# Optimization experiments

Hardware: AMD Instinct MI355X
Metric: run time of the kernel (lower is better)

Reference implementation:

```python
import jax, jax.numpy as jnp
import numpy as np

HEADS = 8
DIM_HEAD = 64
SCALE = DIM_HEAD ** -0.5


def setup_inputs() -> dict:
    key = jax.random.key(0)
    ks = jax.random.split(key, 6)
    B, N, M = 4, 4096, 1024
    QD, CD, ID = 320, 768, 512
    s = lambda d: (1.0 / np.sqrt(d)).astype(np.float32)
    return {
        "x": jax.random.normal(ks[0], (B, N, QD), dtype=jnp.float32),
        "context": jax.random.normal(ks[1], (B, M, CD), dtype=jnp.float32),
        "Wq": jax.random.normal(ks[2], (QD, ID), dtype=jnp.float32) * s(QD),
        "Wk": jax.random.normal(ks[3], (CD, ID), dtype=jnp.float32) * s(CD),
        "Wv": jax.random.normal(ks[4], (CD, ID), dtype=jnp.float32) * s(CD),
        "Wo": jax.random.normal(ks[5], (ID, QD), dtype=jnp.float32) * s(ID),
        "bo": jnp.zeros((QD,), dtype=jnp.float32),
    }


def reference(x, context, Wq, Wk, Wv, Wo, bo):
    B, N, _ = x.shape
    M = context.shape[1]
    # projections
    q = (x @ Wq).reshape(B, N, HEADS, DIM_HEAD)        # b n h d
    k = (context @ Wk).reshape(B, M, HEADS, DIM_HEAD)  # b m h d
    v = (context @ Wv).reshape(B, M, HEADS, DIM_HEAD)
    # scaled dot-product attention per head
    scores = jnp.einsum("bnhd,bmhd->bhnm", q, k) * SCALE
    attn = jax.nn.softmax(scores, axis=-1)
    out = jnp.einsum("bhnm,bmhd->bnhd", attn, v).reshape(B, N, HEADS * DIM_HEAD)
    # output projection (dropout p=0.0 is identity)
    return out @ Wo + bo
```

## Files before the change

### kernel.cpp

```cpp
#include <hip/hip_runtime.h>
#include <cmath>

constexpr int BATCH  = 4;
constexpr int SEQ_N  = 4096;
constexpr int SEQ_M  = 1024;
constexpr int QD     = 320;
constexpr int CD     = 768;
constexpr int ID     = 512;
constexpr float QFOLD = 0.125f * 1.44269504f;
constexpr float EK2F  = -8.0f * 1.44269504f;

typedef __bf16 bf16x8 __attribute__((ext_vector_type(8)));
typedef __bf16 bf16x4 __attribute__((ext_vector_type(4)));
typedef __bf16 bf16x2 __attribute__((ext_vector_type(2)));
typedef float  f32x4  __attribute__((ext_vector_type(4)));

__device__ __forceinline__ void gload_lds16(const __bf16* g, __bf16* l) {
    __builtin_amdgcn_global_load_lds(
        (const __attribute__((address_space(1))) void*)g,
        (__attribute__((address_space(3))) void*)l, 16, 0, 0);
}

__global__ __launch_bounds__(256)
void cvt_all(const float* __restrict__ x, const float* __restrict__ ctx,
             const float* __restrict__ Wq, const float* __restrict__ Wk,
             const float* __restrict__ Wv, const float* __restrict__ Wo,
             __bf16* __restrict__ xb, __bf16* __restrict__ ctxb,
             __bf16* __restrict__ WqT, __bf16* __restrict__ WkT,
             __bf16* __restrict__ WvT, __bf16* __restrict__ WoT) {
    __shared__ float tile[32][33];
    int bid = blockIdx.x;
    if (bid < 4096) {
        constexpr int NX8 = SEQ_N * BATCH * QD / 8;
        int i = bid * 256 + threadIdx.x;
        const float* s; __bf16* d; int j;
        if (i < NX8) { s = x; d = xb; j = i; }
        else         { s = ctx; d = ctxb; j = i - NX8; }
        const float4* sp = reinterpret_cast<const float4*>(s) + (size_t)j * 2;
        float4 a = sp[0], b = sp[1];
        bf16x8 o = { (__bf16)a.x, (__bf16)a.y, (__bf16)a.z, (__bf16)a.w,
                     (__bf16)b.x, (__bf16)b.y, (__bf16)b.z, (__bf16)b.w };
        reinterpret_cast<bf16x8*>(d)[j] = o;
        return;
    }
    int wb = bid - 4096;
    const float* W; __bf16* WT; int K, N, tid; float scl = 1.0f;
    if (wb < 160)      { W = Wq; WT = WqT; K = 320; N = 512; tid = wb; scl = QFOLD; }
    else if (wb < 544) { W = Wk; WT = WkT; K = 768; N = 512; tid = wb - 160; }
    else if (wb < 928) { W = Wv; WT = WvT; K = 768; N = 512; tid = wb - 544; }
    else               { W = Wo; WT = WoT; K = 512; N = 320; tid = wb - 928; }
    int kt = K / 32;
    int k0 = (tid % kt) * 32, n0 = (tid / kt) * 32;
    int tc = threadIdx.x & 31, tr = threadIdx.x >> 5;
#pragma unroll
    for (int p = 0; p < 4; ++p)
        tile[p * 8 + tr][tc] = W[(size_t)(k0 + p * 8 + tr) * N + n0 + tc];
    __syncthreads();
#pragma unroll
    for (int p = 0; p < 4; ++p)
        WT[(size_t)(n0 + p * 8 + tr) * K + k0 + tc] = (__bf16)(tile[tc][p * 8 + tr] * scl);
}

__global__ __launch_bounds__(256)
void gemm_kv(const __bf16* __restrict__ A, const __bf16* __restrict__ BT,
             __bf16* __restrict__ Kb, __bf16* __restrict__ Vt, int M, int K) {
    __shared__ __attribute__((aligned(16))) __bf16 sA[2][64][64];
    __shared__ __attribute__((aligned(16))) __bf16 sB[2][64][64];

    const int t = threadIdx.x;
    const int wave = t >> 6, lane = t & 63;
    const int q = lane >> 4, c = lane & 15;
    const int wm = wave >> 1, wn = wave & 1;
    const int row0 = blockIdx.x * 64, col0 = blockIdx.y * 64;
    const int srow = lane >> 3, sch = lane & 7;
    const int fch = sch ^ srow;

    auto stage = [&](int buf, int k0) {
#pragma unroll
        for (int i = 0; i < 2; ++i) {
            int r = wave * 16 + i * 8;
            gload_lds16(A + (size_t)(row0 + r + srow) * K + k0 + fch * 8,
                        &sA[buf][r][0] + lane * 8);
            gload_lds16(BT + (size_t)(col0 + r + srow) * K + k0 + fch * 8,
                        &sB[buf][r][0] + lane * 8);
        }
    };

    f32x4 acc[2][2] = {};
    stage(0, 0);
    const int iters = K >> 6;
    for (int it = 0; it < iters; ++it) {
        const int p = it & 1;
        __syncthreads();
        if (it + 1 < iters) stage(p ^ 1, (it + 1) * 64);
#pragma unroll
        for (int ks = 0; ks < 2; ++ks) {
            const int so = ((ks * 4 + q) ^ (c & 7)) * 8;
            bf16x8 am[2], bn[2];
#pragma unroll
            for (int i = 0; i < 2; ++i)
                am[i] = *reinterpret_cast<const bf16x8*>(&sA[p][wm * 32 + i * 16 + c][0] + so);
#pragma unroll
            for (int j = 0; j < 2; ++j)
                bn[j] = *reinterpret_cast<const bf16x8*>(&sB[p][wn * 32 + j * 16 + c][0] + so);
#pragma unroll
            for (int i = 0; i < 2; ++i)
#pragma unroll
                for (int j = 0; j < 2; ++j)
                    acc[i][j] = __builtin_amdgcn_mfma_f32_16x16x32_bf16(bn[j], am[i], acc[i][j], 0, 0, 0);
        }
    }

    if (blockIdx.y < 8) {
#pragma unroll
        for (int i = 0; i < 2; ++i)
#pragma unroll
            for (int j = 0; j < 2; ++j) {
                int mrow = row0 + wm * 32 + i * 16 + c;
                int ncol = col0 + wn * 32 + j * 16 + q * 4;
                bf16x4 v = { (__bf16)acc[i][j][0], (__bf16)acc[i][j][1],
                             (__bf16)acc[i][j][2], (__bf16)acc[i][j][3] };
                *reinterpret_cast<bf16x4*>(&Kb[(size_t)mrow * 512 + ncol]) = v;
            }
    } else {
        __bf16* ldsT = (__bf16*)sA;
        __syncthreads();
#pragma unroll
        for (int i = 0; i < 2; ++i)
#pragma unroll
            for (int j = 0; j < 2; ++j) {
                int ml = wm * 32 + i * 16 + c;
                int dl = wn * 32 + j * 16 + q * 4;
#pragma unroll
                for (int r = 0; r < 4; ++r)
                    ldsT[(dl + r) * 72 + ml] = (__bf16)acc[i][j][r];
            }
        __syncthreads();
        int b = row0 >> 10, m0 = row0 & 1023;
        int h = (col0 - 512) >> 6;
        int d = t >> 2, ch = t & 3;
        __bf16* dst = Vt + (((size_t)((b * 8 + h) * 64 + d)) << 10) + m0 + ch * 16;
        const __bf16* src = &ldsT[d * 72 + ch * 16];
        *reinterpret_cast<bf16x8*>(dst)     = *reinterpret_cast<const bf16x8*>(src);
        *reinterpret_cast<bf16x8*>(dst + 8) = *reinterpret_cast<const bf16x8*>(src + 8);
    }
}

__global__ __launch_bounds__(256, 2)
void flash_attn(const __bf16* __restrict__ xb, const __bf16* __restrict__ WqT,
                const __bf16* __restrict__ Kb, const __bf16* __restrict__ Vt,
                __bf16* __restrict__ AO) {
    __shared__ __attribute__((aligned(16))) __bf16 smem[34816];
    __bf16* sPT = smem + 16384;

    const int t = threadIdx.x;
    const int wave = t >> 6, lane = t & 63;
    const int q = lane >> 4, c = lane & 15;
    const int bh = blockIdx.y;
    const int b = bh >> 3, h = bh & 7;
    const int n0 = blockIdx.x * 256;
    const int srow = lane >> 3, sch = lane & 7;
    const int fch = sch ^ srow;

    f32x4 accQ[4][4] = {};
    {
        __bf16* sX = smem;
        __bf16* sW = smem + 16384;
        for (int k0 = 0; k0 < QD; k0 += 64) {
            __syncthreads();
#pragma unroll
            for (int i = 0; i < 8; ++i) {
                int r = wave * 64 + i * 8;
                gload_lds16(xb + (size_t)(b * SEQ_N + n0 + r + srow) * QD + k0 + fch * 8,
                            sX + r * 64 + lane * 8);
            }
#pragma unroll
            for (int i = 0; i < 2; ++i) {
                int r = wave * 16 + i * 8;
                gload_lds16(WqT + (size_t)(h * 64 + r + srow) * QD + k0 + fch * 8,
                            sW + r * 64 + lane * 8);
            }
            __syncthreads();
#pragma unroll
            for (int ks = 0; ks < 2; ++ks) {
                const int so = ((ks * 4 + q) ^ (c & 7)) * 8;
                bf16x8 aw[4], bx[4];
#pragma unroll
                for (int dt = 0; dt < 4; ++dt)
                    aw[dt] = *reinterpret_cast<const bf16x8*>(sW + (dt * 16 + c) * 64 + so);
#pragma unroll
                for (int qt = 0; qt < 4; ++qt)
                    bx[qt] = *reinterpret_cast<const bf16x8*>(sX + (wave * 64 + qt * 16 + c) * 64 + so);
#pragma unroll
                for (int dt = 0; dt < 4; ++dt)
#pragma unroll
                    for (int qt = 0; qt < 4; ++qt)
                        accQ[dt][qt] = __builtin_amdgcn_mfma_f32_16x16x32_bf16(aw[dt], bx[qt], accQ[dt][qt], 0, 0, 0);
            }
        }
    }
    __syncthreads();

    __bf16* sQw = sPT + wave * 4608;
#pragma unroll
    for (int dt = 0; dt < 4; ++dt)
#pragma unroll
        for (int qt = 0; qt < 4; ++qt) {
            bf16x2 w0 = { (__bf16)accQ[dt][qt][0], (__bf16)accQ[dt][qt][1] };
            bf16x2 w1 = { (__bf16)accQ[dt][qt][2], (__bf16)accQ[dt][qt][3] };
            __bf16* pr = sQw + (qt * 16 + c) * 72 + dt * 16 + q * 4;
            *reinterpret_cast<bf16x2*>(pr)     = w0;
            *reinterpret_cast<bf16x2*>(pr + 2) = w1;
        }
    bf16x8 aq[4][2];
#pragma unroll
    for (int qt = 0; qt < 4; ++qt)
#pragma unroll
        for (int ks = 0; ks < 2; ++ks)
            aq[qt][ks] = *reinterpret_cast<const bf16x8*>(sQw + (qt * 16 + c) * 72 + ks * 32 + q * 8);

    auto stageKV = [&](int buf, int m0) {
        __bf16* sK = smem + buf * 8192;
        __bf16* sV = smem + buf * 8192 + 4096;
#pragma unroll
        for (int i = 0; i < 2; ++i) {
            int r = wave * 16 + i * 8;
            gload_lds16(Kb + (size_t)(b * SEQ_M + m0 + r + srow) * ID + h * 64 + fch * 8,
                        sK + r * 64 + lane * 8);
            gload_lds16(Vt + (((size_t)((b * 8 + h) * 64 + r + srow)) << 10) + m0 + fch * 8,
                        sV + r * 64 + lane * 8);
        }
    };

    const bf16x8 ONES = { (__bf16)1.0f, (__bf16)1.0f, (__bf16)1.0f, (__bf16)1.0f,
                          (__bf16)1.0f, (__bf16)1.0f, (__bf16)1.0f, (__bf16)1.0f };
    f32x4 accO[4][4] = {};
    f32x4 accL[4] = {};

    stageKV(0, 0);
    constexpr int TILES = SEQ_M / 64;
    for (int mt = 0; mt < TILES; ++mt) {
        const int p = mt & 1;
        __syncthreads();
        if (mt + 1 < TILES) stageKV(p ^ 1, (mt + 1) * 64);
        const __bf16* sK = smem + p * 8192;
        const __bf16* sV = smem + p * 8192 + 4096;

        f32x4 s[4][4];
#pragma unroll
        for (int qt = 0; qt < 4; ++qt)
#pragma unroll
            for (int ct = 0; ct < 4; ++ct)
                s[qt][ct] = f32x4{ EK2F, EK2F, EK2F, EK2F };
#pragma unroll
        for (int ks = 0; ks < 2; ++ks) {
            const int so = ((ks * 4 + q) ^ (c & 7)) * 8;
#pragma unroll
            for (int ct = 0; ct < 4; ++ct) {
                bf16x8 ak = *reinterpret_cast<const bf16x8*>(sK + (ct * 16 + c) * 64 + so);
#pragma unroll
                for (int qt = 0; qt < 4; ++qt)
                    s[qt][ct] = __builtin_amdgcn_mfma_f32_16x16x32_bf16(ak, aq[qt][ks], s[qt][ct], 0, 0, 0);
            }
        }

#pragma unroll
        for (int qt = 0; qt < 4; ++qt)
#pragma unroll
            for (int ct = 0; ct < 4; ++ct) {
                float p0 = exp2f(s[qt][ct][0]);
                float p1 = exp2f(s[qt][ct][1]);
                float p2 = exp2f(s[qt][ct][2]);
                float p3 = exp2f(s[qt][ct][3]);
                bf16x2 w0 = { (__bf16)p0, (__bf16)p1 };
                bf16x2 w1 = { (__bf16)p2, (__bf16)p3 };
                __bf16* pr = sQw + (qt * 16 + c) * 72 + ct * 16 + q * 4;
                *reinterpret_cast<bf16x2*>(pr)     = w0;
                *reinterpret_cast<bf16x2*>(pr + 2) = w1;
            }

#pragma unroll
        for (int ks = 0; ks < 2; ++ks) {
            const int so = ((ks * 4 + q) ^ (c & 7)) * 8;
            bf16x8 bp[4];
#pragma unroll
            for (int qt = 0; qt < 4; ++qt)
                bp[qt] = *reinterpret_cast<const bf16x8*>(sQw + (qt * 16 + c) * 72 + ks * 32 + q * 8);
#pragma unroll
            for (int qt = 0; qt < 4; ++qt)
                accL[qt] = __builtin_amdgcn_mfma_f32_16x16x32_bf16(ONES, bp[qt], accL[qt], 0, 0, 0);
#pragma unroll
            for (int nt = 0; nt < 4; ++nt) {
                bf16x8 av = *reinterpret_cast<const bf16x8*>(sV + (nt * 16 + c) * 64 + so);
#pragma unroll
                for (int qt = 0; qt < 4; ++qt)
                    accO[qt][nt] = __builtin_amdgcn_mfma_f32_16x16x32_bf16(av, bp[qt], accO[qt][nt], 0, 0, 0);
            }
        }
    }

#pragma unroll
    for (int qt = 0; qt < 4; ++qt) {
        float inv = 1.0f / accL[qt][0];
        size_t rowb = (size_t)(b * SEQ_N + n0 + wave * 64 + qt * 16 + c) * ID + h * 64;
#pragma unroll
        for (int nt = 0; nt < 4; ++nt) {
            bf16x4 v = { (__bf16)(accO[qt][nt][0] * inv), (__bf16)(accO[qt][nt][1] * inv),
                         (__bf16)(accO[qt][nt][2] * inv), (__bf16)(accO[qt][nt][3] * inv) };
            *reinterpret_cast<bf16x4*>(&AO[rowb + nt * 16 + q * 4]) = v;
        }
    }
}

__global__ __launch_bounds__(256)
void gemm_out(const __bf16* __restrict__ A, const __bf16* __restrict__ BT,
              const float* __restrict__ bias, float* __restrict__ C,
              int M, int N, int K) {
    __shared__ __attribute__((aligned(16))) __bf16 sA[2][128][64];
    __shared__ __attribute__((aligned(16))) __bf16 sB[2][64][64];

    const int t = threadIdx.x;
    const int wave = t >> 6, lane = t & 63;
    const int q = lane >> 4, c = lane & 15;
    const int wm = wave >> 1, wn = wave & 1;
    const int row0 = blockIdx.x * 128, col0 = blockIdx.y * 64;
    const int srow = lane >> 3, sch = lane & 7;
    const int fch = sch ^ srow;

    auto stage = [&](int buf, int k0) {
#pragma unroll
        for (int i = 0; i < 4; ++i) {
            int r = wave * 32 + i * 8;
            gload_lds16(A + (size_t)(row0 + r + srow) * K + k0 + fch * 8,
                        &sA[buf][r][0] + lane * 8);
        }
#pragma unroll
        for (int i = 0; i < 2; ++i) {
            int r = wave * 16 + i * 8;
            gload_lds16(BT + (size_t)(col0 + r + srow) * K + k0 + fch * 8,
                        &sB[buf][r][0] + lane * 8);
        }
    };

    f32x4 acc[4][2] = {};
    stage(0, 0);
    const int iters = K >> 6;
    for (int it = 0; it < iters; ++it) {
        const int p = it & 1;
        __syncthreads();
        if (it + 1 < iters) stage(p ^ 1, (it + 1) * 64);
#pragma unroll
        for (int ks = 0; ks < 2; ++ks) {
            const int so = ((ks * 4 + q) ^ (c & 7)) * 8;
            bf16x8 am[4], bn[2];
#pragma unroll
            for (int i = 0; i < 4; ++i)
                am[i] = *reinterpret_cast<const bf16x8*>(&sA[p][wm * 64 + i * 16 + c][0] + so);
#pragma unroll
            for (int j = 0; j < 2; ++j)
                bn[j] = *reinterpret_cast<const bf16x8*>(&sB[p][wn * 32 + j * 16 + c][0] + so);
#pragma unroll
            for (int i = 0; i < 4; ++i)
#pragma unroll
                for (int j = 0; j < 2; ++j)
                    acc[i][j] = __builtin_amdgcn_mfma_f32_16x16x32_bf16(bn[j], am[i], acc[i][j], 0, 0, 0);
        }
    }

#pragma unroll
    for (int i = 0; i < 4; ++i)
#pragma unroll
        for (int j = 0; j < 2; ++j) {
            int mrow = row0 + wm * 64 + i * 16 + c;
            int ncol = col0 + wn * 32 + j * 16 + q * 4;
            float4 v = { acc[i][j][0] + bias[ncol + 0],
                         acc[i][j][1] + bias[ncol + 1],
                         acc[i][j][2] + bias[ncol + 2],
                         acc[i][j][3] + bias[ncol + 3] };
            *reinterpret_cast<float4*>(&C[(size_t)mrow * N + ncol]) = v;
        }
}

extern "C" void kernel_launch(void* const* d_in, const int* in_sizes, int n_in,
                              void* d_out, int out_size, void* d_ws, size_t ws_size,
                              hipStream_t stream) {
    const float* x   = (const float*)d_in[0];
    const float* ctx = (const float*)d_in[1];
    const float* Wq  = (const float*)d_in[2];
    const float* Wk  = (const float*)d_in[3];
    const float* Wv  = (const float*)d_in[4];
    const float* Wo  = (const float*)d_in[5];
    const float* bo  = (const float*)d_in[6];
    float* out = (float*)d_out;

    char* ws = (char*)d_ws;
    __bf16* xb   = (__bf16*)(ws + 0);
    __bf16* ctxb = (__bf16*)(ws + 10485760);
    __bf16* AO   = (__bf16*)(ws + 16777216);
    __bf16* Kb   = (__bf16*)(ws + 33554432);
    __bf16* Vt   = (__bf16*)(ws + 37748736);
    __bf16* WqT  = (__bf16*)(ws + 41943040);
    __bf16* WkT  = (__bf16*)(ws + 42270720);
    __bf16* WvT  = (__bf16*)(ws + 43057152);
    __bf16* WoT  = (__bf16*)(ws + 43843584);

    const int MX = BATCH * SEQ_N;
    const int MC = BATCH * SEQ_M;
    dim3 blk(256);

    cvt_all<<<dim3(5184), blk, 0, stream>>>(x, ctx, Wq, Wk, Wv, Wo,
                                            xb, ctxb, WqT, WkT, WvT, WoT);

    gemm_kv<<<dim3(MC / 64, 16), blk, 0, stream>>>(ctxb, WkT, Kb, Vt, MC, CD);

    flash_attn<<<dim3(SEQ_N / 256, 32), blk, 0, stream>>>(xb, WqT, Kb, Vt, AO);

    gemm_out<<<dim3(MX / 128, QD / 64), blk, 0, stream>>>(AO, WoT, bo, out, MX, QD, ID);
}
```

Before: 173.7 us.

## Shrink flash-attention blocks to two waves and enlarge KV GEMM tiles

gemm_kv moves from 64x64 to 128x128 tiles with 4x4 accumulators per wave, and its V transpose is now done per wave in LDS. flash_attn now runs 128 threads covering 128 query rows, with a smaller LDS footprint. It drops KV double buffering for a single buffer with syncs around each load, and processes the KV tile in two 32-column halves so the P buffer is narrower. The aim is more resident blocks and better latency hiding from lower LDS use, at the cost of losing the overlap of KV loads with compute. Q projection work per block is also duplicated across more blocks.

```diff
diff --git a/kernel.cpp b/kernel.cpp
--- a/kernel.cpp
+++ b/kernel.cpp
@@ -64,21 +64,21 @@
 __global__ __launch_bounds__(256)
 void gemm_kv(const __bf16* __restrict__ A, const __bf16* __restrict__ BT,
              __bf16* __restrict__ Kb, __bf16* __restrict__ Vt, int M, int K) {
-    __shared__ __attribute__((aligned(16))) __bf16 sA[2][64][64];
-    __shared__ __attribute__((aligned(16))) __bf16 sB[2][64][64];
+    __shared__ __attribute__((aligned(16))) __bf16 sA[2][128][64];
+    __shared__ __attribute__((aligned(16))) __bf16 sB[2][128][64];
 
     const int t = threadIdx.x;
     const int wave = t >> 6, lane = t & 63;
     const int q = lane >> 4, c = lane & 15;
     const int wm = wave >> 1, wn = wave & 1;
-    const int row0 = blockIdx.x * 64, col0 = blockIdx.y * 64;
+    const int row0 = blockIdx.x * 128, col0 = blockIdx.y * 128;
     const int srow = lane >> 3, sch = lane & 7;
     const int fch = sch ^ srow;
 
     auto stage = [&](int buf, int k0) {
 #pragma unroll
-        for (int i = 0; i < 2; ++i) {
-            int r = wave * 16 + i * 8;
+        for (int i = 0; i < 4; ++i) {
+            int r = wave * 32 + i * 8;
             gload_lds16(A + (size_t)(row0 + r + srow) * K + k0 + fch * 8,
                         &sA[buf][r][0] + lane * 8);
             gload_lds16(BT + (size_t)(col0 + r + srow) * K + k0 + fch * 8,
@@ -86,7 +86,7 @@
         }
     };
 
-    f32x4 acc[2][2] = {};
+    f32x4 acc[4][4] = {};
     stage(0, 0);
     const int iters = K >> 6;
     for (int it = 0; it < iters; ++it) {
@@ -96,76 +96,82 @@
 #pragma unroll
         for (int ks = 0; ks < 2; ++ks) {
             const int so = ((ks * 4 + q) ^ (c & 7)) * 8;
-            bf16x8 am[2], bn[2];
-#pragma unroll
-            for (int i = 0; i < 2; ++i)
-                am[i] = *reinterpret_cast<const bf16x8*>(&sA[p][wm * 32 + i * 16 + c][0] + so);
-#pragma unroll
-            for (int j = 0; j < 2; ++j)
-                bn[j] = *reinterpret_cast<const bf16x8*>(&sB[p][wn * 32 + j * 16 + c][0] + so);
-#pragma unroll
-            for (int i = 0; i < 2; ++i)
-#pragma unroll
-                for (int j = 0; j < 2; ++j)
+            bf16x8 am[4], bn[4];
+#pragma unroll
+            for (int i = 0; i < 4; ++i)
+                am[i] = *reinterpret_cast<const bf16x8*>(&sA[p][wm * 64 + i * 16 + c][0] + so);
+#pragma unroll
+            for (int j = 0; j < 4; ++j)
+                bn[j] = *reinterpret_cast<const bf16x8*>(&sB[p][wn * 64 + j * 16 + c][0] + so);
+#pragma unroll
+            for (int i = 0; i < 4; ++i)
+#pragma unroll
+                for (int j = 0; j < 4; ++j)
                     acc[i][j] = __builtin_amdgcn_mfma_f32_16x16x32_bf16(bn[j], am[i], acc[i][j], 0, 0, 0);
         }
     }
 
-    if (blockIdx.y < 8) {
-#pragma unroll
-        for (int i = 0; i < 2; ++i)
-#pragma unroll
-            for (int j = 0; j < 2; ++j) {
-                int mrow = row0 + wm * 32 + i * 16 + c;
-                int ncol = col0 + wn * 32 + j * 16 + q * 4;
+    if (blockIdx.y < 4) {
+#pragma unroll
+        for (int i = 0; i < 4; ++i)
+#pragma unroll
+            for (int j = 0; j < 4; ++j) {
+                int mrow = row0 + wm * 64 + i * 16 + c;
+                int ncol = col0 + wn * 64 + j * 16 + q * 4;
                 bf16x4 v = { (__bf16)acc[i][j][0], (__bf16)acc[i][j][1],
                              (__bf16)acc[i][j][2], (__bf16)acc[i][j][3] };
                 *reinterpret_cast<bf16x4*>(&Kb[(size_t)mrow * 512 + ncol]) = v;
             }
     } else {
-        __bf16* ldsT = (__bf16*)sA;
         __syncthreads();
-#pragma unroll
-        for (int i = 0; i < 2; ++i)
-#pragma unroll
-            for (int j = 0; j < 2; ++j) {
-                int ml = wm * 32 + i * 16 + c;
-                int dl = wn * 32 + j * 16 + q * 4;
+        __bf16* ldsT = ((__bf16*)sA) + wave * 4608;
+#pragma unroll
+        for (int i = 0; i < 4; ++i)
+#pragma unroll
+            for (int j = 0; j < 4; ++j)
 #pragma unroll
                 for (int r = 0; r < 4; ++r)
-                    ldsT[(dl + r) * 72 + ml] = (__bf16)acc[i][j][r];
-            }
-        __syncthreads();
-        int b = row0 >> 10, m0 = row0 & 1023;
-        int h = (col0 - 512) >> 6;
-        int d = t >> 2, ch = t & 3;
-        __bf16* dst = Vt + (((size_t)((b * 8 + h) * 64 + d)) << 10) + m0 + ch * 16;
-        const __bf16* src = &ldsT[d * 72 + ch * 16];
-        *reinterpret_cast<bf16x8*>(dst)     = *reinterpret_cast<const bf16x8*>(src);
-        *reinterpret_cast<bf16x8*>(dst + 8) = *reinterpret_cast<const bf16x8*>(src + 8);
-    }
-}
-
-__global__ __launch_bounds__(256, 2)
+                    ldsT[(j * 16 + q * 4 + r) * 72 + i * 16 + c] = (__bf16)acc[i][j][r];
+        int b = row0 >> 10;
+        int mcol = (row0 & 1023) + wm * 64;
+        int dbase = col0 - 512 + wn * 64;
+#pragma unroll
+        for (int it = 0; it < 8; ++it) {
+            int dloc = it * 8 + (lane >> 3);
+            int ch = lane & 7;
+            int dg = dbase + dloc;
+            int h = dg >> 6, d = dg & 63;
+            *reinterpret_cast<bf16x8*>(
+                Vt + (((size_t)((b * 8 + h) * 64 + d)) << 10) + mcol + ch * 8) =
+                *reinterpret_cast<const bf16x8*>(&ldsT[dloc * 72 + ch * 8]);
+        }
+    }
+}
+
+__global__ __launch_bounds__(128, 2)
 void flash_attn(const __bf16* __restrict__ xb, const __bf16* __restrict__ WqT,
                 const __bf16* __restrict__ Kb, const __bf16* __restrict__ Vt,
                 __bf16* __restrict__ AO) {
-    __shared__ __attribute__((aligned(16))) __bf16 smem[34816];
-    __bf16* sPT = smem + 16384;
+    __shared__ __attribute__((aligned(16))) __bf16 smem[13312];
+    __bf16* sK  = smem;
+    __bf16* sV  = smem + 4096;
+    __bf16* sPT = smem + 8192;
 
     const int t = threadIdx.x;
     const int wave = t >> 6, lane = t & 63;
     const int q = lane >> 4, c = lane & 15;
     const int bh = blockIdx.y;
     const int b = bh >> 3, h = bh & 7;
-    const int n0 = blockIdx.x * 256;
+    const int n0 = blockIdx.x * 128;
     const int srow = lane >> 3, sch = lane & 7;
     const int fch = sch ^ srow;
+
+    __bf16* sQw = sPT + wave * 2560;
 
     f32x4 accQ[4][4] = {};
     {
         __bf16* sX = smem;
-        __bf16* sW = smem + 16384;
+        __bf16* sW = smem + 8192;
         for (int k0 = 0; k0 < QD; k0 += 64) {
             __syncthreads();
 #pragma unroll
@@ -175,8 +181,8 @@
                             sX + r * 64 + lane * 8);
             }
 #pragma unroll
-            for (int i = 0; i < 2; ++i) {
-                int r = wave * 16 + i * 8;
+            for (int i = 0; i < 4; ++i) {
+                int r = wave * 32 + i * 8;
                 gload_lds16(WqT + (size_t)(h * 64 + r + srow) * QD + k0 + fch * 8,
                             sW + r * 64 + lane * 8);
             }
@@ -201,30 +207,30 @@
     }
     __syncthreads();
 
-    __bf16* sQw = sPT + wave * 4608;
-#pragma unroll
-    for (int dt = 0; dt < 4; ++dt)
-#pragma unroll
-        for (int qt = 0; qt < 4; ++qt) {
-            bf16x2 w0 = { (__bf16)accQ[dt][qt][0], (__bf16)accQ[dt][qt][1] };
-            bf16x2 w1 = { (__bf16)accQ[dt][qt][2], (__bf16)accQ[dt][qt][3] };
-            __bf16* pr = sQw + (qt * 16 + c) * 72 + dt * 16 + q * 4;
-            *reinterpret_cast<bf16x2*>(pr)     = w0;
-            *reinterpret_cast<bf16x2*>(pr + 2) = w1;
-        }
     bf16x8 aq[4][2];
 #pragma unroll
-    for (int qt = 0; qt < 4; ++qt)
-#pragma unroll
-        for (int ks = 0; ks < 2; ++ks)
-            aq[qt][ks] = *reinterpret_cast<const bf16x8*>(sQw + (qt * 16 + c) * 72 + ks * 32 + q * 8);
-
-    auto stageKV = [&](int buf, int m0) {
-        __bf16* sK = smem + buf * 8192;
-        __bf16* sV = smem + buf * 8192 + 4096;
-#pragma unroll
-        for (int i = 0; i < 2; ++i) {
-            int r = wave * 16 + i * 8;
+    for (int ks = 0; ks < 2; ++ks) {
+#pragma unroll
+        for (int cti = 0; cti < 2; ++cti) {
+            int dt = ks * 2 + cti;
+#pragma unroll
+            for (int qt = 0; qt < 4; ++qt) {
+                bf16x2 w0 = { (__bf16)accQ[dt][qt][0], (__bf16)accQ[dt][qt][1] };
+                bf16x2 w1 = { (__bf16)accQ[dt][qt][2], (__bf16)accQ[dt][qt][3] };
+                __bf16* pr = sQw + (qt * 16 + c) * 40 + cti * 16 + q * 4;
+                *reinterpret_cast<bf16x2*>(pr)     = w0;
+                *reinterpret_cast<bf16x2*>(pr + 2) = w1;
+            }
+        }
+#pragma unroll
+        for (int qt = 0; qt < 4; ++qt)
+            aq[qt][ks] = *reinterpret_cast<const bf16x8*>(sQw + (qt * 16 + c) * 40 + q * 8);
+    }
+
+    auto stageKV = [&](int m0) {
+#pragma unroll
+        for (int i = 0; i < 4; ++i) {
+            int r = wave * 32 + i * 8;
             gload_lds16(Kb + (size_t)(b * SEQ_M + m0 + r + srow) * ID + h * 64 + fch * 8,
                         sK + r * 64 + lane * 8);
             gload_lds16(Vt + (((size_t)((b * 8 + h) * 64 + r + srow)) << 10) + m0 + fch * 8,
@@ -237,61 +243,56 @@
     f32x4 accO[4][4] = {};
     f32x4 accL[4] = {};
 
-    stageKV(0, 0);
-    constexpr int TILES = SEQ_M / 64;
-    for (int mt = 0; mt < TILES; ++mt) {
-        const int p = mt & 1;
+    for (int m0 = 0; m0 < SEQ_M; m0 += 64) {
         __syncthreads();
-        if (mt + 1 < TILES) stageKV(p ^ 1, (mt + 1) * 64);
-        const __bf16* sK = smem + p * 8192;
-        const __bf16* sV = smem + p * 8192 + 4096;
-
-        f32x4 s[4][4];
-#pragma unroll
-        for (int qt = 0; qt < 4; ++qt)
-#pragma unroll
-            for (int ct = 0; ct < 4; ++ct)
-                s[qt][ct] = f32x4{ EK2F, EK2F, EK2F, EK2F };
-#pragma unroll
-        for (int ks = 0; ks < 2; ++ks) {
-            const int so = ((ks * 4 + q) ^ (c & 7)) * 8;
-#pragma unroll
-            for (int ct = 0; ct < 4; ++ct) {
-                bf16x8 ak = *reinterpret_cast<const bf16x8*>(sK + (ct * 16 + c) * 64 + so);
-#pragma unroll
-                for (int qt = 0; qt < 4; ++qt)
-                    s[qt][ct] = __builtin_amdgcn_mfma_f32_16x16x32_bf16(ak, aq[qt][ks], s[qt][ct], 0, 0, 0);
-            }
-        }
-
-#pragma unroll
-        for (int qt = 0; qt < 4; ++qt)
-#pragma unroll
-            for (int ct = 0; ct < 4; ++ct) {
-                float p0 = exp2f(s[qt][ct][0]);
-                float p1 = exp2f(s[qt][ct][1]);
-                float p2 = exp2f(s[qt][ct][2]);
-                float p3 = exp2f(s[qt][ct][3]);
-                bf16x2 w0 = { (__bf16)p0, (__bf16)p1 };
-                bf16x2 w1 = { (__bf16)p2, (__bf16)p3 };
-                __bf16* pr = sQw + (qt * 16 + c) * 72 + ct * 16 + q * 4;
-                *reinterpret_cast<bf16x2*>(pr)     = w0;
-                *reinterpret_cast<bf16x2*>(pr + 2) = w1;
-            }
-
-#pragma unroll
-        for (int ks = 0; ks < 2; ++ks) {
-            const int so = ((ks * 4 + q) ^ (c & 7)) * 8;
+        stageKV(m0);
+        __syncthreads();
+
+#pragma unroll
+        for (int hh = 0; hh < 2; ++hh) {
+            f32x4 s[4][2];
+#pragma unroll
+            for (int qt = 0; qt < 4; ++qt)
+#pragma unroll
+                for (int cti = 0; cti < 2; ++cti)
+                    s[qt][cti] = f32x4{ EK2F, EK2F, EK2F, EK2F };
+#pragma unroll
+            for (int ks = 0; ks < 2; ++ks) {
+                const int so = ((ks * 4 + q) ^ (c & 7)) * 8;
+#pragma unroll
+                for (int cti = 0; cti < 2; ++cti) {
+                    bf16x8 ak = *reinterpret_cast<const bf16x8*>(
+                        sK + ((hh * 2 + cti) * 16 + c) * 64 + so);
+#pragma unroll
+                    for (int qt = 0; qt < 4; ++qt)
+                        s[qt][cti] = __builtin_amdgcn_mfma_f32_16x16x32_bf16(ak, aq[qt][ks], s[qt][cti], 0, 0, 0);
+                }
+            }
+#pragma unroll
+            for (int qt = 0; qt < 4; ++qt)
+#pragma unroll
+                for (int cti = 0; cti < 2; ++cti) {
+                    float p0 = exp2f(s[qt][cti][0]);
+                    float p1 = exp2f(s[qt][cti][1]);
+                    float p2 = exp2f(s[qt][cti][2]);
+                    float p3 = exp2f(s[qt][cti][3]);
+                    bf16x2 w0 = { (__bf16)p0, (__bf16)p1 };
+                    bf16x2 w1 = { (__bf16)p2, (__bf16)p3 };
+                    __bf16* pr = sQw + (qt * 16 + c) * 40 + cti * 16 + q * 4;
+                    *reinterpret_cast<bf16x2*>(pr)     = w0;
+                    *reinterpret_cast<bf16x2*>(pr + 2) = w1;
+                }
+            const int soh = ((hh * 4 + q) ^ (c & 7)) * 8;
             bf16x8 bp[4];
 #pragma unroll
             for (int qt = 0; qt < 4; ++qt)
-                bp[qt] = *reinterpret_cast<const bf16x8*>(sQw + (qt * 16 + c) * 72 + ks * 32 + q * 8);
+                bp[qt] = *reinterpret_cast<const bf16x8*>(sQw + (qt * 16 + c) * 40 + q * 8);
 #pragma unroll
             for (int qt = 0; qt < 4; ++qt)
                 accL[qt] = __builtin_amdgcn_mfma_f32_16x16x32_bf16(ONES, bp[qt], accL[qt], 0, 0, 0);
 #pragma unroll
             for (int nt = 0; nt < 4; ++nt) {
-                bf16x8 av = *reinterpret_cast<const bf16x8*>(sV + (nt * 16 + c) * 64 + so);
+                bf16x8 av = *reinterpret_cast<const bf16x8*>(sV + (nt * 16 + c) * 64 + soh);
 #pragma unroll
                 for (int qt = 0; qt < 4; ++qt)
                     accO[qt][nt] = __builtin_amdgcn_mfma_f32_16x16x32_bf16(av, bp[qt], accO[qt][nt], 0, 0, 0);
@@ -406,14 +407,13 @@
 
     const int MX = BATCH * SEQ_N;
     const int MC = BATCH * SEQ_M;
-    dim3 blk(256);
-
-    cvt_all<<<dim3(5184), blk, 0, stream>>>(x, ctx, Wq, Wk, Wv, Wo,
-                                            xb, ctxb, WqT, WkT, WvT, WoT);
-
-    gemm_kv<<<dim3(MC / 64, 16), blk, 0, stream>>>(ctxb, WkT, Kb, Vt, MC, CD);
-
-    flash_attn<<<dim3(SEQ_N / 256, 32), blk, 0, stream>>>(xb, WqT, Kb, Vt, AO);
-
-    gemm_out<<<dim3(MX / 128, QD / 64), blk, 0, stream>>>(AO, WoT, bo, out, MX, QD, ID);
-}
+
+    cvt_all<<<dim3(5184), dim3(256), 0, stream>>>(x, ctx, Wq, Wk, Wv, Wo,
+                                                  xb, ctxb, WqT, WkT, WvT, WoT);
+
+    gemm_kv<<<dim3(MC / 128, 8), dim3(256), 0, stream>>>(ctxb, WkT, Kb, Vt, MC, CD);
+
+    flash_attn<<<dim3(SEQ_N / 128, 32), dim3(128), 0, stream>>>(xb, WqT, Kb, Vt, AO);
+
+    gemm_out<<<dim3(MX / 128, QD / 64), dim3(256), 0, stream>>>(AO, WoT, bo, out, MX, QD, ID);
+}
```

Result: slower. 182.8 us (+5.2%).

## Split attention KV range across wave pairs with smaller query tiles

Applied to the files above, without the earlier changes.

The flash attention block now covers 128 queries instead of 256. Its four waves form two query halves by two key halves, each pair handling half of every 64-key tile and merging partial outputs and row sums through LDS at the end. Row sums are now computed with scalar adds and shuffles instead of a ones-vector MFMA. The K/V staging is split by role (two waves load K, two load a swizzled V), and launch bounds request 3 blocks per CU with less shared memory. The aim is more blocks and better occupancy, at the cost of an extra LDS reduction, more synchronisation, and recomputing the Q projection twice as often per key stream.

```diff
diff --git a/kernel.cpp b/kernel.cpp
--- a/kernel.cpp
+++ b/kernel.cpp
@@ -12,7 +12,6 @@
 
 typedef __bf16 bf16x8 __attribute__((ext_vector_type(8)));
 typedef __bf16 bf16x4 __attribute__((ext_vector_type(4)));
-typedef __bf16 bf16x2 __attribute__((ext_vector_type(2)));
 typedef float  f32x4  __attribute__((ext_vector_type(4)));
 
 __device__ __forceinline__ void gload_lds16(const __bf16* g, __bf16* l) {
@@ -146,53 +145,53 @@
     }
 }
 
-__global__ __launch_bounds__(256, 2)
+__global__ __launch_bounds__(256, 3)
 void flash_attn(const __bf16* __restrict__ xb, const __bf16* __restrict__ WqT,
                 const __bf16* __restrict__ Kb, const __bf16* __restrict__ Vt,
                 __bf16* __restrict__ AO) {
-    __shared__ __attribute__((aligned(16))) __bf16 smem[34816];
-    __bf16* sPT = smem + 16384;
+    __shared__ __attribute__((aligned(16))) __bf16 smem[26624];
 
     const int t = threadIdx.x;
     const int wave = t >> 6, lane = t & 63;
     const int q = lane >> 4, c = lane & 15;
+    const int qh = wave & 1, kh = wave >> 1;
     const int bh = blockIdx.y;
     const int b = bh >> 3, h = bh & 7;
-    const int n0 = blockIdx.x * 256;
+    const int n0 = blockIdx.x * 128;
     const int srow = lane >> 3, sch = lane & 7;
     const int fch = sch ^ srow;
 
-    f32x4 accQ[4][4] = {};
+    f32x4 accQ[2][4] = {};
     {
         __bf16* sX = smem;
-        __bf16* sW = smem + 16384;
+        __bf16* sW = smem + 8192;
         for (int k0 = 0; k0 < QD; k0 += 64) {
             __syncthreads();
 #pragma unroll
-            for (int i = 0; i < 8; ++i) {
-                int r = wave * 64 + i * 8;
-                gload_lds16(xb + (size_t)(b * SEQ_N + n0 + r + srow) * QD + k0 + fch * 8,
-                            sX + r * 64 + lane * 8);
+            for (int i = 0; i < 4; ++i) {
+                int r = wave * 32 + i * 8 + srow;
+                gload_lds16(xb + (size_t)(b * SEQ_N + n0 + r) * QD + k0 + fch * 8,
+                            sX + (wave * 32 + i * 8) * 64 + lane * 8);
             }
 #pragma unroll
             for (int i = 0; i < 2; ++i) {
-                int r = wave * 16 + i * 8;
-                gload_lds16(WqT + (size_t)(h * 64 + r + srow) * QD + k0 + fch * 8,
-                            sW + r * 64 + lane * 8);
+                int r = wave * 16 + i * 8 + srow;
+                gload_lds16(WqT + (size_t)(h * 64 + r) * QD + k0 + fch * 8,
+                            sW + (wave * 16 + i * 8) * 64 + lane * 8);
             }
             __syncthreads();
 #pragma unroll
             for (int ks = 0; ks < 2; ++ks) {
                 const int so = ((ks * 4 + q) ^ (c & 7)) * 8;
-                bf16x8 aw[4], bx[4];
-#pragma unroll
-                for (int dt = 0; dt < 4; ++dt)
-                    aw[dt] = *reinterpret_cast<const bf16x8*>(sW + (dt * 16 + c) * 64 + so);
+                bf16x8 aw[2], bx[4];
+#pragma unroll
+                for (int dt = 0; dt < 2; ++dt)
+                    aw[dt] = *reinterpret_cast<const bf16x8*>(sW + (kh * 32 + dt * 16 + c) * 64 + so);
 #pragma unroll
                 for (int qt = 0; qt < 4; ++qt)
-                    bx[qt] = *reinterpret_cast<const bf16x8*>(sX + (wave * 64 + qt * 16 + c) * 64 + so);
-#pragma unroll
-                for (int dt = 0; dt < 4; ++dt)
+                    bx[qt] = *reinterpret_cast<const bf16x8*>(sX + (qh * 64 + qt * 16 + c) * 64 + so);
+#pragma unroll
+                for (int dt = 0; dt < 2; ++dt)
 #pragma unroll
                     for (int qt = 0; qt < 4; ++qt)
                         accQ[dt][qt] = __builtin_amdgcn_mfma_f32_16x16x32_bf16(aw[dt], bx[qt], accQ[dt][qt], 0, 0, 0);
@@ -200,63 +199,72 @@
         }
     }
     __syncthreads();
-
-    __bf16* sQw = sPT + wave * 4608;
-#pragma unroll
-    for (int dt = 0; dt < 4; ++dt)
+    __bf16* sQ = smem + 16384;
+#pragma unroll
+    for (int dt = 0; dt < 2; ++dt)
 #pragma unroll
         for (int qt = 0; qt < 4; ++qt) {
-            bf16x2 w0 = { (__bf16)accQ[dt][qt][0], (__bf16)accQ[dt][qt][1] };
-            bf16x2 w1 = { (__bf16)accQ[dt][qt][2], (__bf16)accQ[dt][qt][3] };
-            __bf16* pr = sQw + (qt * 16 + c) * 72 + dt * 16 + q * 4;
-            *reinterpret_cast<bf16x2*>(pr)     = w0;
-            *reinterpret_cast<bf16x2*>(pr + 2) = w1;
-        }
+            bf16x4 v = { (__bf16)accQ[dt][qt][0], (__bf16)accQ[dt][qt][1],
+                         (__bf16)accQ[dt][qt][2], (__bf16)accQ[dt][qt][3] };
+            *reinterpret_cast<bf16x4*>(sQ + (qh * 64 + qt * 16 + c) * 72 + kh * 32 + dt * 16 + q * 4) = v;
+        }
+    __syncthreads();
     bf16x8 aq[4][2];
 #pragma unroll
     for (int qt = 0; qt < 4; ++qt)
 #pragma unroll
         for (int ks = 0; ks < 2; ++ks)
-            aq[qt][ks] = *reinterpret_cast<const bf16x8*>(sQw + (qt * 16 + c) * 72 + ks * 32 + q * 8);
-
-    auto stageKV = [&](int buf, int m0) {
-        __bf16* sK = smem + buf * 8192;
-        __bf16* sV = smem + buf * 8192 + 4096;
-#pragma unroll
-        for (int i = 0; i < 2; ++i) {
-            int r = wave * 16 + i * 8;
-            gload_lds16(Kb + (size_t)(b * SEQ_M + m0 + r + srow) * ID + h * 64 + fch * 8,
-                        sK + r * 64 + lane * 8);
-            gload_lds16(Vt + (((size_t)((b * 8 + h) * 64 + r + srow)) << 10) + m0 + fch * 8,
-                        sV + r * 64 + lane * 8);
+            aq[qt][ks] = *reinterpret_cast<const bf16x8*>(sQ + (qh * 64 + qt * 16 + c) * 72 + ks * 32 + q * 8);
+    __syncthreads();
+
+    auto stageKV = [&](int p, int m0) {
+        __bf16* sK = smem + p * 8192;
+        __bf16* sV = smem + p * 8192 + 4096;
+        if (wave < 2) {
+#pragma unroll
+            for (int i = 0; i < 4; ++i) {
+                int r = wave * 32 + i * 8 + srow;
+                int mg = (r >> 5) * 512 + m0 + (r & 31);
+                gload_lds16(Kb + (size_t)(b * SEQ_M + mg) * ID + h * 64 + fch * 8,
+                            sK + (wave * 32 + i * 8) * 64 + lane * 8);
+            }
+        } else {
+            int v = wave - 2;
+            int sr2 = lane >> 2, sc2 = lane & 3;
+#pragma unroll
+            for (int i = 0; i < 4; ++i) {
+                int rr = v * 64 + i * 16 + sr2;
+                int d = rr & 63, st = rr >> 6;
+                int f2 = sc2 ^ ((rr >> 1) & 3);
+                gload_lds16(Vt + (((size_t)((b * 8 + h) * 64 + d)) << 10) + st * 512 + m0 + f2 * 8,
+                            sV + (v * 64 + i * 16) * 32 + lane * 8);
+            }
         }
     };
 
-    const bf16x8 ONES = { (__bf16)1.0f, (__bf16)1.0f, (__bf16)1.0f, (__bf16)1.0f,
-                          (__bf16)1.0f, (__bf16)1.0f, (__bf16)1.0f, (__bf16)1.0f };
     f32x4 accO[4][4] = {};
-    f32x4 accL[4] = {};
+    float l4[4] = {};
+    __bf16* sPTw = smem + 16384 + wave * 2560;
 
     stageKV(0, 0);
-    constexpr int TILES = SEQ_M / 64;
-    for (int mt = 0; mt < TILES; ++mt) {
+    for (int mt = 0; mt < 16; ++mt) {
         const int p = mt & 1;
         __syncthreads();
-        if (mt + 1 < TILES) stageKV(p ^ 1, (mt + 1) * 64);
-        const __bf16* sK = smem + p * 8192;
-        const __bf16* sV = smem + p * 8192 + 4096;
-
-        f32x4 s[4][4];
+        if (mt + 1 < 16) stageKV(p ^ 1, (mt + 1) * 32);
+        const __bf16* sK = smem + p * 8192 + kh * 2048;
+        const __bf16* sV = smem + p * 8192 + 4096 + kh * 2048;
+
+        f32x4 s[4][2];
 #pragma unroll
         for (int qt = 0; qt < 4; ++qt)
 #pragma unroll
-            for (int ct = 0; ct < 4; ++ct)
+            for (int ct = 0; ct < 2; ++ct)
                 s[qt][ct] = f32x4{ EK2F, EK2F, EK2F, EK2F };
 #pragma unroll
         for (int ks = 0; ks < 2; ++ks) {
             const int so = ((ks * 4 + q) ^ (c & 7)) * 8;
 #pragma unroll
-            for (int ct = 0; ct < 4; ++ct) {
+            for (int ct = 0; ct < 2; ++ct) {
                 bf16x8 ak = *reinterpret_cast<const bf16x8*>(sK + (ct * 16 + c) * 64 + so);
 #pragma unroll
                 for (int qt = 0; qt < 4; ++qt)
@@ -267,47 +275,67 @@
 #pragma unroll
         for (int qt = 0; qt < 4; ++qt)
 #pragma unroll
-            for (int ct = 0; ct < 4; ++ct) {
+            for (int ct = 0; ct < 2; ++ct) {
                 float p0 = exp2f(s[qt][ct][0]);
                 float p1 = exp2f(s[qt][ct][1]);
                 float p2 = exp2f(s[qt][ct][2]);
                 float p3 = exp2f(s[qt][ct][3]);
-                bf16x2 w0 = { (__bf16)p0, (__bf16)p1 };
-                bf16x2 w1 = { (__bf16)p2, (__bf16)p3 };
-                __bf16* pr = sQw + (qt * 16 + c) * 72 + ct * 16 + q * 4;
-                *reinterpret_cast<bf16x2*>(pr)     = w0;
-                *reinterpret_cast<bf16x2*>(pr + 2) = w1;
-            }
-
-#pragma unroll
-        for (int ks = 0; ks < 2; ++ks) {
-            const int so = ((ks * 4 + q) ^ (c & 7)) * 8;
-            bf16x8 bp[4];
+                l4[qt] += (p0 + p1) + (p2 + p3);
+                bf16x4 w = { (__bf16)p0, (__bf16)p1, (__bf16)p2, (__bf16)p3 };
+                *reinterpret_cast<bf16x4*>(sPTw + (qt * 16 + c) * 40 + ct * 16 + q * 4) = w;
+            }
+
+        const int sov = (q ^ ((c >> 1) & 3)) * 8;
+        bf16x8 bp[4];
+#pragma unroll
+        for (int qt = 0; qt < 4; ++qt)
+            bp[qt] = *reinterpret_cast<const bf16x8*>(sPTw + (qt * 16 + c) * 40 + q * 8);
+#pragma unroll
+        for (int nt = 0; nt < 4; ++nt) {
+            bf16x8 av = *reinterpret_cast<const bf16x8*>(sV + (nt * 16 + c) * 32 + sov);
 #pragma unroll
             for (int qt = 0; qt < 4; ++qt)
-                bp[qt] = *reinterpret_cast<const bf16x8*>(sQw + (qt * 16 + c) * 72 + ks * 32 + q * 8);
+                accO[qt][nt] = __builtin_amdgcn_mfma_f32_16x16x32_bf16(av, bp[qt], accO[qt][nt], 0, 0, 0);
+        }
+    }
+
+#pragma unroll
+    for (int qt = 0; qt < 4; ++qt) {
+        l4[qt] += __shfl_xor(l4[qt], 16, 64);
+        l4[qt] += __shfl_xor(l4[qt], 32, 64);
+    }
+    __syncthreads();
+    float* dO = (float*)smem;
+    float* dL = (float*)smem + 8192;
+    if (kh == 1) {
+#pragma unroll
+        for (int qt = 0; qt < 4; ++qt)
+#pragma unroll
+            for (int nt = 0; nt < 4; ++nt)
+#pragma unroll
+                for (int r = 0; r < 4; ++r)
+                    dO[qh * 4096 + qt * 1024 + (nt * 16 + q * 4 + r) * 16 + c] = accO[qt][nt][r];
+        if (q == 0)
 #pragma unroll
             for (int qt = 0; qt < 4; ++qt)
-                accL[qt] = __builtin_amdgcn_mfma_f32_16x16x32_bf16(ONES, bp[qt], accL[qt], 0, 0, 0);
+                dL[qh * 64 + qt * 16 + c] = l4[qt];
+    }
+    __syncthreads();
+    if (kh == 0) {
+#pragma unroll
+        for (int qt = 0; qt < 4; ++qt) {
+            float inv = 1.0f / (l4[qt] + dL[qh * 64 + qt * 16 + c]);
+            size_t rowb = (size_t)(b * SEQ_N + n0 + qh * 64 + qt * 16 + c) * ID + h * 64;
 #pragma unroll
             for (int nt = 0; nt < 4; ++nt) {
-                bf16x8 av = *reinterpret_cast<const bf16x8*>(sV + (nt * 16 + c) * 64 + so);
-#pragma unroll
-                for (int qt = 0; qt < 4; ++qt)
-                    accO[qt][nt] = __builtin_amdgcn_mfma_f32_16x16x32_bf16(av, bp[qt], accO[qt][nt], 0, 0, 0);
-            }
-        }
-    }
-
-#pragma unroll
-    for (int qt = 0; qt < 4; ++qt) {
-        float inv = 1.0f / accL[qt][0];
-        size_t rowb = (size_t)(b * SEQ_N + n0 + wave * 64 + qt * 16 + c) * ID + h * 64;
-#pragma unroll
-        for (int nt = 0; nt < 4; ++nt) {
-            bf16x4 v = { (__bf16)(accO[qt][nt][0] * inv), (__bf16)(accO[qt][nt][1] * inv),
-                         (__bf16)(accO[qt][nt][2] * inv), (__bf16)(accO[qt][nt][3] * inv) };
-            *reinterpret_cast<bf16x4*>(&AO[rowb + nt * 16 + q * 4]) = v;
+                float o0 = accO[qt][nt][0] + dO[qh * 4096 + qt * 1024 + (nt * 16 + q * 4 + 0) * 16 + c];
+                float o1 = accO[qt][nt][1] + dO[qh * 4096 + qt * 1024 + (nt * 16 + q * 4 + 1) * 16 + c];
+                float o2 = accO[qt][nt][2] + dO[qh * 4096 + qt * 1024 + (nt * 16 + q * 4 + 2) * 16 + c];
+                float o3 = accO[qt][nt][3] + dO[qh * 4096 + qt * 1024 + (nt * 16 + q * 4 + 3) * 16 + c];
+                bf16x4 v = { (__bf16)(o0 * inv), (__bf16)(o1 * inv),
+                             (__bf16)(o2 * inv), (__bf16)(o3 * inv) };
+                *reinterpret_cast<bf16x4*>(&AO[rowb + nt * 16 + q * 4]) = v;
+            }
         }
     }
 }
@@ -406,14 +434,13 @@
 
     const int MX = BATCH * SEQ_N;
     const int MC = BATCH * SEQ_M;
-    dim3 blk(256);
-
-    cvt_all<<<dim3(5184), blk, 0, stream>>>(x, ctx, Wq, Wk, Wv, Wo,
-                                            xb, ctxb, WqT, WkT, WvT, WoT);
-
-    gemm_kv<<<dim3(MC / 64, 16), blk, 0, stream>>>(ctxb, WkT, Kb, Vt, MC, CD);
-
-    flash_attn<<<dim3(SEQ_N / 256, 32), blk, 0, stream>>>(xb, WqT, Kb, Vt, AO);
-
-    gemm_out<<<dim3(MX / 128, QD / 64), blk, 0, stream>>>(AO, WoT, bo, out, MX, QD, ID);
-}
+
+    cvt_all<<<dim3(5184), dim3(256), 0, stream>>>(x, ctx, Wq, Wk, Wv, Wo,
+                                                  xb, ctxb, WqT, WkT, WvT, WoT);
+
+    gemm_kv<<<dim3(MC / 64, 16), dim3(256), 0, stream>>>(ctxb, WkT, Kb, Vt, MC, CD);
+
+    flash_attn<<<dim3(SEQ_N / 128, 32), dim3(256), 0, stream>>>(xb, WqT, Kb, Vt, AO);
+
+    gemm_out<<<dim3(MX / 128, QD / 64), dim3(256), 0, stream>>>(AO, WoT, bo, out, MX, QD, ID);
+}
```

New measurement: 227.8 us. 1.31x slower.

## Split attention over two key halves and combine partials in output GEMM

Applied to the files above, without the earlier changes.

Flash attention now launches a second grid dimension that processes half of the context keys each, writing unnormalized bf16 partial outputs and row sums to separate buffers. The output projection GEMM loads both partials, sums them, and normalizes them while staging A into shared memory. The KV staging becomes single-buffered with less LDS, and occupancy is raised to 3 blocks per CU, aiming to fill more CUs. In exchange, the Q projection is computed twice, the partial outputs add global memory traffic, and KV load latency is no longer overlapped.

```diff
diff --git a/kernel.cpp b/kernel.cpp
--- a/kernel.cpp
+++ b/kernel.cpp
@@ -146,12 +146,13 @@
     }
 }
 
-__global__ __launch_bounds__(256, 2)
+__global__ __launch_bounds__(256, 3)
 void flash_attn(const __bf16* __restrict__ xb, const __bf16* __restrict__ WqT,
                 const __bf16* __restrict__ Kb, const __bf16* __restrict__ Vt,
-                __bf16* __restrict__ AO) {
-    __shared__ __attribute__((aligned(16))) __bf16 smem[34816];
-    __bf16* sPT = smem + 16384;
+                __bf16* __restrict__ AO0, __bf16* __restrict__ AO1,
+                float* __restrict__ L0, float* __restrict__ L1) {
+    __shared__ __attribute__((aligned(16))) __bf16 smem[26624];
+    __bf16* sPT = smem + 8192;
 
     const int t = threadIdx.x;
     const int wave = t >> 6, lane = t & 63;
@@ -159,8 +160,12 @@
     const int bh = blockIdx.y;
     const int b = bh >> 3, h = bh & 7;
     const int n0 = blockIdx.x * 256;
+    const int ks2 = blockIdx.z;
     const int srow = lane >> 3, sch = lane & 7;
     const int fch = sch ^ srow;
+
+    __bf16* AOp = ks2 ? AO1 : AO0;
+    float*  Lp  = ks2 ? L1  : L0;
 
     f32x4 accQ[4][4] = {};
     {
@@ -182,8 +187,8 @@
             }
             __syncthreads();
 #pragma unroll
-            for (int ks = 0; ks < 2; ++ks) {
-                const int so = ((ks * 4 + q) ^ (c & 7)) * 8;
+            for (int ksi = 0; ksi < 2; ++ksi) {
+                const int so = ((ksi * 4 + q) ^ (c & 7)) * 8;
                 bf16x8 aw[4], bx[4];
 #pragma unroll
                 for (int dt = 0; dt < 4; ++dt)
@@ -216,19 +221,17 @@
 #pragma unroll
     for (int qt = 0; qt < 4; ++qt)
 #pragma unroll
-        for (int ks = 0; ks < 2; ++ks)
-            aq[qt][ks] = *reinterpret_cast<const bf16x8*>(sQw + (qt * 16 + c) * 72 + ks * 32 + q * 8);
-
-    auto stageKV = [&](int buf, int m0) {
-        __bf16* sK = smem + buf * 8192;
-        __bf16* sV = smem + buf * 8192 + 4096;
+        for (int ksi = 0; ksi < 2; ++ksi)
+            aq[qt][ksi] = *reinterpret_cast<const bf16x8*>(sQw + (qt * 16 + c) * 72 + ksi * 32 + q * 8);
+
+    auto stageKV = [&](int m0) {
 #pragma unroll
         for (int i = 0; i < 2; ++i) {
             int r = wave * 16 + i * 8;
             gload_lds16(Kb + (size_t)(b * SEQ_M + m0 + r + srow) * ID + h * 64 + fch * 8,
-                        sK + r * 64 + lane * 8);
+                        smem + r * 64 + lane * 8);
             gload_lds16(Vt + (((size_t)((b * 8 + h) * 64 + r + srow)) << 10) + m0 + fch * 8,
-                        sV + r * 64 + lane * 8);
+                        smem + 4096 + r * 64 + lane * 8);
         }
     };
 
@@ -237,14 +240,14 @@
     f32x4 accO[4][4] = {};
     f32x4 accL[4] = {};
 
-    stageKV(0, 0);
-    constexpr int TILES = SEQ_M / 64;
-    for (int mt = 0; mt < TILES; ++mt) {
-        const int p = mt & 1;
-        __syncthreads();
-        if (mt + 1 < TILES) stageKV(p ^ 1, (mt + 1) * 64);
-        const __bf16* sK = smem + p * 8192;
-        const __bf16* sV = smem + p * 8192 + 4096;
+    const __bf16* sK = smem;
+    const __bf16* sV = smem + 4096;
+
+    for (int mt = 0; mt < 8; ++mt) {
+        const int m0 = ks2 * 512 + mt * 64;
+        __syncthreads();
+        stageKV(m0);
+        __syncthreads();
 
         f32x4 s[4][4];
 #pragma unroll
@@ -253,14 +256,14 @@
             for (int ct = 0; ct < 4; ++ct)
                 s[qt][ct] = f32x4{ EK2F, EK2F, EK2F, EK2F };
 #pragma unroll
-        for (int ks = 0; ks < 2; ++ks) {
-            const int so = ((ks * 4 + q) ^ (c & 7)) * 8;
+        for (int ksi = 0; ksi < 2; ++ksi) {
+            const int so = ((ksi * 4 + q) ^ (c & 7)) * 8;
 #pragma unroll
             for (int ct = 0; ct < 4; ++ct) {
                 bf16x8 ak = *reinterpret_cast<const bf16x8*>(sK + (ct * 16 + c) * 64 + so);
 #pragma unroll
                 for (int qt = 0; qt < 4; ++qt)
-                    s[qt][ct] = __builtin_amdgcn_mfma_f32_16x16x32_bf16(ak, aq[qt][ks], s[qt][ct], 0, 0, 0);
+                    s[qt][ct] = __builtin_amdgcn_mfma_f32_16x16x32_bf16(ak, aq[qt][ksi], s[qt][ct], 0, 0, 0);
             }
         }
 
@@ -280,12 +283,12 @@
             }
 
 #pragma unroll
-        for (int ks = 0; ks < 2; ++ks) {
-            const int so = ((ks * 4 + q) ^ (c & 7)) * 8;
+        for (int ksi = 0; ksi < 2; ++ksi) {
+            const int so = ((ksi * 4 + q) ^ (c & 7)) * 8;
             bf16x8 bp[4];
 #pragma unroll
             for (int qt = 0; qt < 4; ++qt)
-                bp[qt] = *reinterpret_cast<const bf16x8*>(sQw + (qt * 16 + c) * 72 + ks * 32 + q * 8);
+                bp[qt] = *reinterpret_cast<const bf16x8*>(sQw + (qt * 16 + c) * 72 + ksi * 32 + q * 8);
 #pragma unroll
             for (int qt = 0; qt < 4; ++qt)
                 accL[qt] = __builtin_amdgcn_mfma_f32_16x16x32_bf16(ONES, bp[qt], accL[qt], 0, 0, 0);
@@ -301,21 +304,24 @@
 
 #pragma unroll
     for (int qt = 0; qt < 4; ++qt) {
-        float inv = 1.0f / accL[qt][0];
-        size_t rowb = (size_t)(b * SEQ_N + n0 + wave * 64 + qt * 16 + c) * ID + h * 64;
+        int row = n0 + wave * 64 + qt * 16 + c;
+        if (q == 0)
+            Lp[(size_t)(b * SEQ_N + row) * 8 + h] = accL[qt][0];
+        size_t rowb = (size_t)(b * SEQ_N + row) * ID + h * 64;
 #pragma unroll
         for (int nt = 0; nt < 4; ++nt) {
-            bf16x4 v = { (__bf16)(accO[qt][nt][0] * inv), (__bf16)(accO[qt][nt][1] * inv),
-                         (__bf16)(accO[qt][nt][2] * inv), (__bf16)(accO[qt][nt][3] * inv) };
-            *reinterpret_cast<bf16x4*>(&AO[rowb + nt * 16 + q * 4]) = v;
+            bf16x4 v = { (__bf16)accO[qt][nt][0], (__bf16)accO[qt][nt][1],
+                         (__bf16)accO[qt][nt][2], (__bf16)accO[qt][nt][3] };
+            *reinterpret_cast<bf16x4*>(&AOp[rowb + nt * 16 + q * 4]) = v;
         }
     }
 }
 
 __global__ __launch_bounds__(256)
-void gemm_out(const __bf16* __restrict__ A, const __bf16* __restrict__ BT,
-              const float* __restrict__ bias, float* __restrict__ C,
-              int M, int N, int K) {
+void gemm_out(const __bf16* __restrict__ AO0, const __bf16* __restrict__ AO1,
+              const float* __restrict__ L0, const float* __restrict__ L1,
+              const __bf16* __restrict__ BT, const float* __restrict__ bias,
+              float* __restrict__ C, int M, int N, int K) {
     __shared__ __attribute__((aligned(16))) __bf16 sA[2][128][64];
     __shared__ __attribute__((aligned(16))) __bf16 sB[2][64][64];
 
@@ -327,13 +333,28 @@
     const int srow = lane >> 3, sch = lane & 7;
     const int fch = sch ^ srow;
 
-    auto stage = [&](int buf, int k0) {
+    auto loadA = [&](int k0, bf16x8 a0[4], bf16x8 a1[4], float inv[4]) {
+        int h = k0 >> 6;
 #pragma unroll
         for (int i = 0; i < 4; ++i) {
-            int r = wave * 32 + i * 8;
-            gload_lds16(A + (size_t)(row0 + r + srow) * K + k0 + fch * 8,
-                        &sA[buf][r][0] + lane * 8);
-        }
+            int r = row0 + wave * 32 + i * 8 + srow;
+            size_t off = (size_t)r * K + k0 + fch * 8;
+            a0[i] = *reinterpret_cast<const bf16x8*>(AO0 + off);
+            a1[i] = *reinterpret_cast<const bf16x8*>(AO1 + off);
+            inv[i] = 1.0f / (L0[(size_t)r * 8 + h] + L1[(size_t)r * 8 + h]);
+        }
+    };
+    auto writeA = [&](int buf, bf16x8 a0[4], bf16x8 a1[4], float inv[4]) {
+#pragma unroll
+        for (int i = 0; i < 4; ++i) {
+            bf16x8 o;
+#pragma unroll
+            for (int e = 0; e < 8; ++e)
+                o[e] = (__bf16)(((float)a0[i][e] + (float)a1[i][e]) * inv[i]);
+            *reinterpret_cast<bf16x8*>(&sA[buf][wave * 32 + i * 8][0] + lane * 8) = o;
+        }
+    };
+    auto stageB = [&](int buf, int k0) {
 #pragma unroll
         for (int i = 0; i < 2; ++i) {
             int r = wave * 16 + i * 8;
@@ -343,15 +364,24 @@
     };
 
     f32x4 acc[4][2] = {};
-    stage(0, 0);
+    {
+        bf16x8 a0[4], a1[4]; float inv[4];
+        loadA(0, a0, a1, inv);
+        writeA(0, a0, a1, inv);
+        stageB(0, 0);
+    }
     const int iters = K >> 6;
     for (int it = 0; it < iters; ++it) {
         const int p = it & 1;
         __syncthreads();
-        if (it + 1 < iters) stage(p ^ 1, (it + 1) * 64);
-#pragma unroll
-        for (int ks = 0; ks < 2; ++ks) {
-            const int so = ((ks * 4 + q) ^ (c & 7)) * 8;
+        bf16x8 na0[4], na1[4]; float ninv[4];
+        if (it + 1 < iters) {
+            loadA((it + 1) * 64, na0, na1, ninv);
+            stageB(p ^ 1, (it + 1) * 64);
+        }
+#pragma unroll
+        for (int ksi = 0; ksi < 2; ++ksi) {
+            const int so = ((ksi * 4 + q) ^ (c & 7)) * 8;
             bf16x8 am[4], bn[2];
 #pragma unroll
             for (int i = 0; i < 4; ++i)
@@ -365,6 +395,7 @@
                 for (int j = 0; j < 2; ++j)
                     acc[i][j] = __builtin_amdgcn_mfma_f32_16x16x32_bf16(bn[j], am[i], acc[i][j], 0, 0, 0);
         }
+        if (it + 1 < iters) writeA(p ^ 1, na0, na1, ninv);
     }
 
 #pragma unroll
@@ -396,24 +427,28 @@
     char* ws = (char*)d_ws;
     __bf16* xb   = (__bf16*)(ws + 0);
     __bf16* ctxb = (__bf16*)(ws + 10485760);
-    __bf16* AO   = (__bf16*)(ws + 16777216);
+    __bf16* AO0  = (__bf16*)(ws + 16777216);
     __bf16* Kb   = (__bf16*)(ws + 33554432);
     __bf16* Vt   = (__bf16*)(ws + 37748736);
     __bf16* WqT  = (__bf16*)(ws + 41943040);
     __bf16* WkT  = (__bf16*)(ws + 42270720);
     __bf16* WvT  = (__bf16*)(ws + 43057152);
     __bf16* WoT  = (__bf16*)(ws + 43843584);
+    __bf16* AO1  = (__bf16*)(ws + 44171264);
+    float*  L0   = (float*)(ws + 60948480);
+    float*  L1   = (float*)(ws + 61472768);
 
     const int MX = BATCH * SEQ_N;
     const int MC = BATCH * SEQ_M;
-    dim3 blk(256);
-
-    cvt_all<<<dim3(5184), blk, 0, stream>>>(x, ctx, Wq, Wk, Wv, Wo,
-                                            xb, ctxb, WqT, WkT, WvT, WoT);
-
-    gemm_kv<<<dim3(MC / 64, 16), blk, 0, stream>>>(ctxb, WkT, Kb, Vt, MC, CD);
-
-    flash_attn<<<dim3(SEQ_N / 256, 32), blk, 0, stream>>>(xb, WqT, Kb, Vt, AO);
-
-    gemm_out<<<dim3(MX / 128, QD / 64), blk, 0, stream>>>(AO, WoT, bo, out, MX, QD, ID);
-}
+
+    cvt_all<<<dim3(5184), dim3(256), 0, stream>>>(x, ctx, Wq, Wk, Wv, Wo,
+                                                  xb, ctxb, WqT, WkT, WvT, WoT);
+
+    gemm_kv<<<dim3(MC / 64, 16), dim3(256), 0, stream>>>(ctxb, WkT, Kb, Vt, MC, CD);
+
+    flash_attn<<<dim3(SEQ_N / 256, 32, 2), dim3(256), 0, stream>>>(
+        xb, WqT, Kb, Vt, AO0, AO1, L0, L1);
+
+    gemm_out<<<dim3(MX / 128, QD / 64), dim3(256), 0, stream>>>(
+        AO0, AO1, L0, L1, WoT, bo, out, MX, QD, ID);
+}
```

Measured after the change: 280.0 us. +61.2%, slower.
